# Kernel tuning notes

Measured on AMD Instinct MI355X. Metric: run time of the kernel, lower is better.

Reference implementation:

```python
import jax, jax.numpy as jnp
import numpy as np

D = 1024
HEADS = 16
HD = D // HEADS


def setup_inputs() -> dict:
    key = jax.random.key(0)
    kx, kqkv, kout = jax.random.split(key, 3)
    x = jax.random.normal(kx, (2, 2048, D), dtype=jnp.float32)
    # torch Linear weight is [out, in]; store same layout
    W_qkv = jax.random.normal(kqkv, (3 * D, D), dtype=jnp.float32) * (D ** -0.5)
    W_out = jax.random.normal(kout, (D, D), dtype=jnp.float32) * (D ** -0.5)
    return {"x": x, "W_qkv": W_qkv, "W_out": W_out}


def reference(x, W_qkv, W_out):
    B, T, _ = x.shape
    scale = HD ** -0.5
    qkv = jnp.einsum('btd,ed->bte', x, W_qkv)            # [B,T,3D]
    qkv = qkv.reshape(B, T, 3, HEADS, HD)
    q = jnp.transpose(qkv[:, :, 0], (0, 2, 1, 3))        # [B,H,T,hd]
    k = jnp.transpose(qkv[:, :, 1], (0, 2, 1, 3))
    v = jnp.transpose(qkv[:, :, 2], (0, 2, 1, 3))
    attn = jnp.einsum('bhqd,bhkd->bhqk', q, k) * scale   # [B,H,T,T]
    causal = jnp.tril(jnp.ones((T, T), dtype=bool))
    attn = jnp.where(causal, attn, -jnp.inf)
    attn = jax.nn.softmax(attn, axis=-1)
    out = jnp.einsum('bhqk,bhkd->bhqd', attn, v)         # [B,H,T,hd]
    out = jnp.transpose(out, (0, 2, 1, 3)).reshape(B, T, HEADS * HD)
    return jnp.einsum('btd,ed->bte', out, W_out)
```

## Files before the change

### kernel.cpp

```cpp
#include <hip/hip_runtime.h>
#include <cmath>


typedef unsigned short u16;
typedef unsigned int u32;
typedef short short8 __attribute__((ext_vector_type(8)));
typedef float floatx4 __attribute__((ext_vector_type(4)));

#define T_SZ 2048
#define HD_SZ 64
#define QSCALE 0.1803368801111244f

__device__ __forceinline__ u16 f2bf(float f) {
  unsigned u = __float_as_uint(f);
  u += 0x7fffu + ((u >> 16) & 1u);
  return (u16)(u >> 16);
}

__device__ __forceinline__ u32 pack_bf2(float lo, float hi) {
  return __builtin_amdgcn_perm(__float_as_uint(hi), __float_as_uint(lo), 0x07060302u);
}

__device__ __forceinline__ u32 cvtpk(float a, float b) {
  u32 r;
  asm("v_cvt_pk_bf16_f32 %0, %1, %2" : "=v"(r) : "v"(a), "v"(b));
  return r;
}

__device__ __forceinline__ void pl32swap(u32& a, u32& b) {
  asm("v_permlane32_swap_b32 %0, %1" : "+v"(a), "+v"(b));
}
__device__ __forceinline__ void pl16swap(u32& a, u32& b) {
  asm("v_permlane16_swap_b32 %0, %1" : "+v"(a), "+v"(b));
}

__device__ __forceinline__ void exp4(float s0, float s1, float s2, float s3,
                                     float& p0, float& p1, float& p2, float& p3) {
  asm("v_exp_f32 %0, %4\n\t"
      "v_exp_f32 %1, %5\n\t"
      "v_exp_f32 %2, %6\n\t"
      "v_exp_f32 %3, %7\n\t"
      "s_nop 1"
      : "=&v"(p0), "=&v"(p1), "=&v"(p2), "=&v"(p3)
      : "v"(s0), "v"(s1), "v"(s2), "v"(s3));
}

__device__ __forceinline__ void gload16(const u16* g, u16* l) {
  __builtin_amdgcn_global_load_lds(
      (const __attribute__((address_space(1))) void*)g,
      (__attribute__((address_space(3))) void*)l, 16, 0, 0);
}

__global__ __launch_bounds__(256) void cast3(const float* __restrict__ a, u16* __restrict__ ao, int na4,
                                             const float* __restrict__ b, u16* __restrict__ bo, int nb4,
                                             const float* __restrict__ c, u16* __restrict__ co, int nc4) {
  int i = blockIdx.x * 256 + threadIdx.x;
  const float* src;
  u16* dst;
  int j;
  if (i < na4) { src = a; dst = ao; j = i; }
  else if (i < na4 + nb4) { src = b; dst = bo; j = i - na4; }
  else { j = i - na4 - nb4; if (j >= nc4) return; src = c; dst = co; }
  float4 f = ((const float4*)src)[j];
  ushort4 o;
  o.x = f2bf(f.x); o.y = f2bf(f.y); o.z = f2bf(f.z); o.w = f2bf(f.w);
  ((ushort4*)dst)[j] = o;
}

__global__ __launch_bounds__(512, 6) void gemm_qkv(const u16* __restrict__ A,
                                                   const u16* __restrict__ Bt,
                                                   u16* __restrict__ Qf,
                                                   u16* __restrict__ Kf,
                                                   u16* __restrict__ Vf) {
  __shared__ u16 SM[4 * 64 * 72];
  u16* As = SM;
  u16* Bs = SM + 128 * 64;
  const int Kdim = 1024;
  const int tid = threadIdx.x;
  const int lane = tid & 63;
  const int wave = tid >> 6;
  const int quad = lane >> 4;
  const int l16 = lane & 15;
  const int wm = wave >> 2;
  const int wn = wave & 3;
  const int linear = blockIdx.y * 24 + blockIdx.x;
  const int nb = (linear & 7) * 96 + (linear >> 3);
  const int bxx = nb % 24;
  const int byy = nb / 24;
  const int m0 = byy * 128;
  const int n0 = bxx * 128;

  floatx4 acc[4][2];
#pragma unroll
  for (int i = 0; i < 4; i++)
#pragma unroll
    for (int j = 0; j < 2; j++) acc[i][j] = (floatx4){0.f, 0.f, 0.f, 0.f};

  const int srow = lane >> 3;
  const int scol = ((lane & 7) ^ srow) * 8;
  const u16* gpA[2];
  const u16* gpB[2];
  u16 *lpA[2], *lpB[2];
#pragma unroll
  for (int u = 0; u < 2; u++) {
    const int row = wave * 16 + u * 8 + srow;
    gpA[u] = A + (size_t)(m0 + row) * Kdim + scol;
    gpB[u] = Bt + (size_t)(n0 + row) * Kdim + scol;
    lpA[u] = As + (wave * 16 + u * 8) * 64 + lane * 8;
    lpB[u] = Bs + (wave * 16 + u * 8) * 64 + lane * 8;
  }

  const int fsw = l16 & 7;

  for (int k0 = 0; k0 < Kdim; k0 += 64) {
    __syncthreads();
#pragma unroll
    for (int u = 0; u < 2; u++) {
      gload16(gpA[u] + k0, lpA[u]);
      gload16(gpB[u] + k0, lpB[u]);
    }
    __syncthreads();

#pragma unroll
    for (int h = 0; h < 2; h++) {
      const int seg = ((h * 4 + quad) ^ fsw) * 8;
      short8 af[4], bf[2];
#pragma unroll
      for (int mt = 0; mt < 4; mt++)
        af[mt] = *(const short8*)&As[(wm * 64 + mt * 16 + l16) * 64 + seg];
#pragma unroll
      for (int nt = 0; nt < 2; nt++)
        bf[nt] = *(const short8*)&Bs[(wn * 32 + nt * 16 + l16) * 64 + seg];
#pragma unroll
      for (int mt = 0; mt < 4; mt++)
#pragma unroll
        for (int nt = 0; nt < 2; nt++)
          acc[mt][nt] = __builtin_amdgcn_mfma_f32_16x16x32_bf16(af[mt], bf[nt], acc[mt][nt], 0, 0, 0);
    }
  }

  const int dest = n0 >> 10;
  const int qn = wn >> 1;
  const int wh = wn & 1;
  const int n0w = n0 + qn * 64;
  const int m_abs = m0 + wm * 64;
  const int b = m_abs >> 11;
  const int t0w = m_abs & 2047;
  const int h = (n0w >> 6) & 15;
  const int bh = b * 16 + h;
  u16* dstp = (dest == 0) ? Qf : (dest == 1) ? Kf : Vf;

  __syncthreads();
  u16* ep = &SM[(wm * 2 + qn) * 64 * 72];
  if (dest == 2) {
#pragma unroll
    for (int nt = 0; nt < 2; nt++) {
#pragma unroll
      for (int mt = 0; mt < 4; mt++) {
        uint2 w;
        w.x = (u32)f2bf(acc[mt][nt][0]) | ((u32)f2bf(acc[mt][nt][1]) << 16);
        w.y = (u32)f2bf(acc[mt][nt][2]) | ((u32)f2bf(acc[mt][nt][3]) << 16);
        *(uint2*)&ep[(wh * 32 + nt * 16 + l16) * 72 + mt * 16 + quad * 4] = w;
      }
    }
  } else {
    const float sc = (dest == 0) ? QSCALE : 1.0f;
#pragma unroll
    for (int mt = 0; mt < 4; mt++)
#pragma unroll
      for (int nt = 0; nt < 2; nt++)
#pragma unroll
        for (int r = 0; r < 4; r++)
          ep[(mt * 16 + quad * 4 + r) * 72 + wh * 32 + nt * 16 + l16] =
              f2bf(acc[mt][nt][r] * sc);
  }
  __syncthreads();
#pragma unroll
  for (int blk = 0; blk < 4; blk++) {
    const int blkk = blk * 2 + wh;
    const int tgd = blkk >> 1;
    const int half = blkk & 1;
    const short8 v = *(const short8*)&ep[(tgd * 16 + l16) * 72 + half * 32 + quad * 8];
    size_t base;
    if (dest == 0)
      base = ((size_t)(bh * 128 + (t0w >> 4) + tgd) * 2 + half) * 512;
    else
      base = (((size_t)(bh * 32 + (t0w >> 6)) * 4 + tgd) * 2 + half) * 512;
    *(short8*)(dstp + base + lane * 8) = v;
  }
}

__global__ __launch_bounds__(512, 4) void gemm_out(const u16* __restrict__ A,
                                                   const u16* __restrict__ Bt,
                                                   float* __restrict__ Cout) {
  __shared__ u16 As[64 * 64];
  __shared__ u16 Bs[128 * 64];
  const int Kdim = 1024;
  const int tid = threadIdx.x;
  const int lane = tid & 63;
  const int wave = tid >> 6;
  const int quad = lane >> 4;
  const int l16 = lane & 15;
  const int wm = wave >> 2;
  const int wn = wave & 3;
  const int linear = blockIdx.y * 8 + blockIdx.x;
  const int nb = (linear & 7) * 64 + (linear >> 3);
  const int m0 = (nb >> 3) * 64;
  const int n0 = (nb & 7) * 128;

  floatx4 acc[2][2];
#pragma unroll
  for (int i = 0; i < 2; i++)
#pragma unroll
    for (int j = 0; j < 2; j++) acc[i][j] = (floatx4){0.f, 0.f, 0.f, 0.f};

  const int srow = lane >> 3;
  const int scol = ((lane & 7) ^ srow) * 8;
  const u16* gpA = A + (size_t)(m0 + wave * 8 + srow) * Kdim + scol;
  u16* lpA = As + (wave * 8) * 64 + lane * 8;
  const u16* gpB[2];
  u16* lpB[2];
#pragma unroll
  for (int u = 0; u < 2; u++) {
    const int row = wave * 16 + u * 8 + srow;
    gpB[u] = Bt + (size_t)(n0 + row) * Kdim + scol;
    lpB[u] = Bs + (wave * 16 + u * 8) * 64 + lane * 8;
  }

  const int fsw = l16 & 7;

  for (int k0 = 0; k0 < Kdim; k0 += 64) {
    __syncthreads();
    gload16(gpA + k0, lpA);
#pragma unroll
    for (int u = 0; u < 2; u++) gload16(gpB[u] + k0, lpB[u]);
    __syncthreads();

#pragma unroll
    for (int h = 0; h < 2; h++) {
      const int seg = ((h * 4 + quad) ^ fsw) * 8;
      short8 af[2], bf[2];
#pragma unroll
      for (int mt = 0; mt < 2; mt++)
        af[mt] = *(const short8*)&As[(wm * 32 + mt * 16 + l16) * 64 + seg];
#pragma unroll
      for (int nt = 0; nt < 2; nt++)
        bf[nt] = *(const short8*)&Bs[(wn * 32 + nt * 16 + l16) * 64 + seg];
#pragma unroll
      for (int mt = 0; mt < 2; mt++)
#pragma unroll
        for (int nt = 0; nt < 2; nt++)
          acc[mt][nt] = __builtin_amdgcn_mfma_f32_16x16x32_bf16(af[mt], bf[nt], acc[mt][nt], 0, 0, 0);
    }
  }

#pragma unroll
  for (int mt = 0; mt < 2; mt++)
#pragma unroll
    for (int nt = 0; nt < 2; nt++)
#pragma unroll
      for (int r = 0; r < 4; r++) {
        const int m = m0 + wm * 32 + mt * 16 + quad * 4 + r;
        const int n = n0 + wn * 32 + nt * 16 + l16;
        Cout[(size_t)m * 1024 + n] = acc[mt][nt][r];
      }
}

__global__ __launch_bounds__(256, 4) void flash_attn(const u16* __restrict__ Qf,
                                                     const u16* __restrict__ Kf,
                                                     const u16* __restrict__ Vf,
                                                     u16* __restrict__ Og) {
  __shared__ __align__(16) u16 KV[2][16 * 512];
  const int tid = threadIdx.x;
  const int lane = tid & 63, wave = tid >> 6;
  const int quad = lane >> 4, l16 = lane & 15;
  const int bh = blockIdx.x;
  const int by = blockIdx.y;
  const int r = by & 7, qq = by >> 3;
  const int g = (qq == 0) ? r : (qq == 1) ? 15 - r : (qq == 2) ? 16 + r : 31 - r;
  const int b = bh >> 4, h = bh & 15;
  const u16* Qb = Qf + ((size_t)bh << 17);
  const u16* Kb = Kf + ((size_t)bh << 17);
  const u16* Vb = Vf + ((size_t)bh << 17);

  const u16* qp = Qb + ((size_t)(g * 4 + wave)) * 1024 + lane * 8;
  const short8 qf0 = *(const short8*)qp;
  const short8 qf1 = *(const short8*)(qp + 512);

  floatx4 l_acc = (floatx4){0.f, 0.f, 0.f, 0.f};
  floatx4 o_acc[4];
#pragma unroll
  for (int dt = 0; dt < 4; dt++) o_acc[dt] = (floatx4){0.f, 0.f, 0.f, 0.f};

  short8 onesf;
#pragma unroll
  for (int i = 0; i < 8; i++) onesf[i] = (short)0x3F80;

  const u16* gkv[4];
  u16* l0[4];
  u16* l1[4];
#pragma unroll
  for (int i = 0; i < 4; i++) {
    const int c = wave * 4 + i;
    gkv[i] = ((c < 8) ? (Kb + c * 512) : (Vb + (c - 8) * 512)) + lane * 8;
    l0[i] = &KV[0][c * 512] + lane * 8;
    l1[i] = &KV[1][c * 512] + lane * 8;
  }

  auto load_tile = [&](int kt, u16* const* lp) {
#pragma unroll
    for (int i = 0; i < 4; i++) gload16(gkv[i] + (size_t)kt * 4096, lp[i]);
  };

  const floatx4 zero4 = {0.f, 0.f, 0.f, 0.f};

  auto compute = [&](int kt, const u16* Kl) {
    const bool diag = (kt == g);
    short8 ka[4][2];
#pragma unroll
    for (int nt = 0; nt < 4; nt++)
#pragma unroll
      for (int hh = 0; hh < 2; hh++)
        ka[nt][hh] = *(const short8*)&Kl[(nt * 2 + hh) * 512 + lane * 8];
    floatx4 sacc[4];
    __builtin_amdgcn_s_setprio(1);
#pragma unroll
    for (int nt = 0; nt < 4; nt++) {
      if (diag && nt > wave) continue;
      floatx4 s = __builtin_amdgcn_mfma_f32_16x16x32_bf16(ka[nt][0], qf0, zero4, 0, 0, 0);
      sacc[nt] = __builtin_amdgcn_mfma_f32_16x16x32_bf16(ka[nt][1], qf1, s, 0, 0, 0);
    }
    __builtin_amdgcn_s_setprio(0);
    u32 c[4][2];
#pragma unroll
    for (int nt = 0; nt < 4; nt++) {
      float p0 = 0.f, p1 = 0.f, p2 = 0.f, p3 = 0.f;
      if (!(diag && nt > wave)) {
        exp4(sacc[nt][0], sacc[nt][1], sacc[nt][2], sacc[nt][3], p0, p1, p2, p3);
        if (diag && nt == wave) {
          if (quad * 4 + 0 > l16) p0 = 0.f;
          if (quad * 4 + 1 > l16) p1 = 0.f;
          if (quad * 4 + 2 > l16) p2 = 0.f;
          if (quad * 4 + 3 > l16) p3 = 0.f;
        }
      }
      c[nt][0] = cvtpk(p0, p1);
      c[nt][1] = cvtpk(p2, p3);
    }
    pl32swap(c[0][0], c[1][0]); pl16swap(c[0][0], c[1][0]);
    pl32swap(c[0][1], c[1][1]); pl16swap(c[0][1], c[1][1]);
    pl32swap(c[2][0], c[3][0]); pl16swap(c[2][0], c[3][0]);
    pl32swap(c[2][1], c[3][1]); pl16swap(c[2][1], c[3][1]);
    union { u32 w[4]; short8 s8; } P0, P1;
    P0.w[0] = c[0][0]; P0.w[1] = c[0][1]; P0.w[2] = c[1][0]; P0.w[3] = c[1][1];
    P1.w[0] = c[2][0]; P1.w[1] = c[2][1]; P1.w[2] = c[3][0]; P1.w[3] = c[3][1];
    const short8 pf0 = P0.s8;
    const short8 pf1 = P1.s8;
    short8 va[4][2];
#pragma unroll
    for (int dt = 0; dt < 4; dt++)
#pragma unroll
      for (int hh = 0; hh < 2; hh++)
        va[dt][hh] = *(const short8*)&Kl[4096 + (dt * 2 + hh) * 512 + lane * 8];
    const bool skip_hi = diag && (wave < 2);
    __builtin_amdgcn_s_setprio(1);
    l_acc = __builtin_amdgcn_mfma_f32_16x16x32_bf16(onesf, pf0, l_acc, 0, 0, 0);
    if (!skip_hi)
      l_acc = __builtin_amdgcn_mfma_f32_16x16x32_bf16(onesf, pf1, l_acc, 0, 0, 0);
#pragma unroll
    for (int dt = 0; dt < 4; dt++) {
      o_acc[dt] = __builtin_amdgcn_mfma_f32_16x16x32_bf16(va[dt][0], pf0, o_acc[dt], 0, 0, 0);
      if (!skip_hi)
        o_acc[dt] = __builtin_amdgcn_mfma_f32_16x16x32_bf16(va[dt][1], pf1, o_acc[dt], 0, 0, 0);
    }
    __builtin_amdgcn_s_setprio(0);
  };

  load_tile(0, l0);
  __syncthreads();
  int kt = 0;
  for (;;) {
    if (kt < g) load_tile(kt + 1, l1);
    compute(kt, &KV[0][0]);
    if (++kt > g) break;
    __syncthreads();
    if (kt < g) load_tile(kt + 1, l0);
    compute(kt, &KV[1][0]);
    if (++kt > g) break;
    __syncthreads();
  }

  const float inv_l = 1.0f / l_acc[0];
  const int t0 = g * 64 + wave * 16;
  const size_t row = ((size_t)(b * 2048 + t0 + l16) << 10) + h * 64;
#pragma unroll
  for (int dt = 0; dt < 4; dt++) {
    uint2 w;
    w.x = pack_bf2(o_acc[dt][0] * inv_l, o_acc[dt][1] * inv_l);
    w.y = pack_bf2(o_acc[dt][2] * inv_l, o_acc[dt][3] * inv_l);
    *(uint2*)&Og[row + dt * 16 + quad * 4] = w;
  }
}

extern "C" void kernel_launch(void* const* d_in, const int* in_sizes, int n_in,
                              void* d_out, int out_size, void* d_ws, size_t ws_size,
                              hipStream_t stream) {
  const float* x = (const float*)d_in[0];
  const float* Wqkv = (const float*)d_in[1];
  const float* Wout = (const float*)d_in[2];
  float* out = (float*)d_out;

  char* ws = (char*)d_ws;
  u16* xb    = (u16*)(ws + 0);
  u16* wqkvb = (u16*)(ws + 8388608);
  u16* woutb = (u16*)(ws + 14680064);
  u16* Qf    = (u16*)(ws + 16777216);
  u16* Kf    = (u16*)(ws + 25165824);
  u16* Vf    = (u16*)(ws + 33554432);
  u16* attn  = (u16*)(ws + 41943040);

  cast3<<<8192, 256, 0, stream>>>(x, xb, 1048576, Wqkv, wqkvb, 786432,
                                  Wout, woutb, 262144);

  gemm_qkv<<<dim3(24, 32), 512, 0, stream>>>(xb, wqkvb, Qf, Kf, Vf);

  flash_attn<<<dim3(32, 32), 256, 0, stream>>>(Qf, Kf, Vf, attn);

  gemm_out<<<dim3(8, 64), 512, 0, stream>>>(attn, woutb, out);
}
```

Baseline: 154.7 us.

## Fuse cast, QKV GEMM, attention and output GEMM into one cooperative kernel

Replaces the four separate launches with a single persistent cooperative kernel of 1024 blocks of 256 threads. The stages are separated by grid.sync and keep the original multi-kernel path as a fallback. The GEMM stages are re-tiled for 256-thread blocks: the QKV GEMM keeps 128x128 tiles spread over 768 blocks, and the output GEMM uses smaller 64x64 tiles. The aim is to remove launch gaps and inter-kernel tail effects. The cost is grid-wide barriers, a 4-blocks-per-CU occupancy requirement, and smaller or different tiles that may lower GEMM efficiency.

```diff
diff --git a/kernel.cpp b/kernel.cpp
--- a/kernel.cpp
+++ b/kernel.cpp
@@ -1,5 +1,8 @@
 #include <hip/hip_runtime.h>
+#include <hip/hip_cooperative_groups.h>
 #include <cmath>
+
+namespace cg = cooperative_groups;
 
 
 typedef unsigned short u16;
@@ -7,8 +10,6 @@
 typedef short short8 __attribute__((ext_vector_type(8)));
 typedef float floatx4 __attribute__((ext_vector_type(4)));
 
-#define T_SZ 2048
-#define HD_SZ 64
 #define QSCALE 0.1803368801111244f
 
 __device__ __forceinline__ u16 f2bf(float f) {
@@ -49,6 +50,352 @@
   __builtin_amdgcn_global_load_lds(
       (const __attribute__((address_space(1))) void*)g,
       (__attribute__((address_space(3))) void*)l, 16, 0, 0);
+}
+
+__global__ __launch_bounds__(256, 4) void fused(const float* __restrict__ x,
+                                                const float* __restrict__ Wqkv,
+                                                const float* __restrict__ Wout,
+                                                u16* __restrict__ xb,
+                                                u16* __restrict__ wqkvb,
+                                                u16* __restrict__ woutb,
+                                                u16* __restrict__ Qf,
+                                                u16* __restrict__ Kf,
+                                                u16* __restrict__ Vf,
+                                                u16* __restrict__ attn,
+                                                float* __restrict__ out) {
+  cg::grid_group grid = cg::this_grid();
+  __shared__ __align__(16) u16 SM[2 * 128 * 64];
+
+  const int tid = threadIdx.x;
+  const int blk = blockIdx.x;
+  const int lane = tid & 63, wave = tid >> 6;
+  const int quad = lane >> 4, l16 = lane & 15;
+  const int srow = lane >> 3;
+  const int scol = ((lane & 7) ^ srow) * 8;
+  const int fsw = l16 & 7;
+
+  {
+    const int na4 = 1048576, nb4 = 786432, nc4 = 262144;
+    const int nTot = na4 + nb4 + nc4;
+    for (int i = blk * 256 + tid; i < nTot; i += 1024 * 256) {
+      const float* src;
+      u16* dst;
+      int j;
+      if (i < na4) { src = x; dst = xb; j = i; }
+      else if (i < na4 + nb4) { src = Wqkv; dst = wqkvb; j = i - na4; }
+      else { src = Wout; dst = woutb; j = i - na4 - nb4; }
+      float4 f = ((const float4*)src)[j];
+      ushort4 o;
+      o.x = f2bf(f.x); o.y = f2bf(f.y); o.z = f2bf(f.z); o.w = f2bf(f.w);
+      ((ushort4*)dst)[j] = o;
+    }
+  }
+  grid.sync();
+
+  if (blk < 768) {
+    u16* As = SM;
+    u16* Bs = SM + 128 * 64;
+    const int Kdim = 1024;
+    const int wm = wave >> 1, wn = wave & 1;
+    const int nb = (blk & 7) * 96 + (blk >> 3);
+    const int bxx = nb % 24;
+    const int byy = nb / 24;
+    const int m0 = byy * 128;
+    const int n0 = bxx * 128;
+
+    floatx4 acc[4][4];
+#pragma unroll
+    for (int i = 0; i < 4; i++)
+#pragma unroll
+      for (int j = 0; j < 4; j++) acc[i][j] = (floatx4){0.f, 0.f, 0.f, 0.f};
+
+    const u16* gpA[4];
+    const u16* gpB[4];
+    u16 *lpA[4], *lpB[4];
+#pragma unroll
+    for (int u = 0; u < 4; u++) {
+      const int row = wave * 32 + u * 8 + srow;
+      gpA[u] = xb + (size_t)(m0 + row) * Kdim + scol;
+      gpB[u] = wqkvb + (size_t)(n0 + row) * Kdim + scol;
+      lpA[u] = As + (wave * 32 + u * 8) * 64 + lane * 8;
+      lpB[u] = Bs + (wave * 32 + u * 8) * 64 + lane * 8;
+    }
+
+    for (int k0 = 0; k0 < Kdim; k0 += 64) {
+      __syncthreads();
+#pragma unroll
+      for (int u = 0; u < 4; u++) {
+        gload16(gpA[u] + k0, lpA[u]);
+        gload16(gpB[u] + k0, lpB[u]);
+      }
+      __syncthreads();
+#pragma unroll
+      for (int h = 0; h < 2; h++) {
+        const int seg = ((h * 4 + quad) ^ fsw) * 8;
+        short8 af[4], bf[4];
+#pragma unroll
+        for (int mt = 0; mt < 4; mt++)
+          af[mt] = *(const short8*)&As[(wm * 64 + mt * 16 + l16) * 64 + seg];
+#pragma unroll
+        for (int nt = 0; nt < 4; nt++)
+          bf[nt] = *(const short8*)&Bs[(wn * 64 + nt * 16 + l16) * 64 + seg];
+#pragma unroll
+        for (int mt = 0; mt < 4; mt++)
+#pragma unroll
+          for (int nt = 0; nt < 4; nt++)
+            acc[mt][nt] = __builtin_amdgcn_mfma_f32_16x16x32_bf16(af[mt], bf[nt], acc[mt][nt], 0, 0, 0);
+      }
+    }
+
+    const int dest = n0 >> 10;
+    const int n0w = n0 + wn * 64;
+    const int m_abs = m0 + wm * 64;
+    const int bb = m_abs >> 11;
+    const int t0w = m_abs & 2047;
+    const int hh_ = (n0w >> 6) & 15;
+    const int bh1 = bb * 16 + hh_;
+    u16* dstp = (dest == 0) ? Qf : (dest == 1) ? Kf : Vf;
+
+    auto do_epi = [&](u16* ep) {
+      if (dest == 2) {
+#pragma unroll
+        for (int nt = 0; nt < 4; nt++) {
+#pragma unroll
+          for (int mt = 0; mt < 4; mt++) {
+            uint2 w;
+            w.x = (u32)f2bf(acc[mt][nt][0]) | ((u32)f2bf(acc[mt][nt][1]) << 16);
+            w.y = (u32)f2bf(acc[mt][nt][2]) | ((u32)f2bf(acc[mt][nt][3]) << 16);
+            *(uint2*)&ep[(nt * 16 + l16) * 72 + mt * 16 + quad * 4] = w;
+          }
+        }
+      } else {
+        const float sc = (dest == 0) ? QSCALE : 1.0f;
+#pragma unroll
+        for (int mt = 0; mt < 4; mt++)
+#pragma unroll
+          for (int nt = 0; nt < 4; nt++)
+#pragma unroll
+            for (int r2 = 0; r2 < 4; r2++)
+              ep[(mt * 16 + quad * 4 + r2) * 72 + nt * 16 + l16] =
+                  f2bf(acc[mt][nt][r2] * sc);
+      }
+#pragma unroll
+      for (int bki = 0; bki < 8; bki++) {
+        const int tgd = bki >> 1;
+        const int half = bki & 1;
+        const short8 v = *(const short8*)&ep[(tgd * 16 + l16) * 72 + half * 32 + quad * 8];
+        size_t base;
+        if (dest == 0)
+          base = ((size_t)(bh1 * 128 + (t0w >> 4) + tgd) * 2 + half) * 512;
+        else
+          base = (((size_t)(bh1 * 32 + (t0w >> 6)) * 4 + tgd) * 2 + half) * 512;
+        *(short8*)(dstp + base + lane * 8) = v;
+      }
+    };
+
+    __syncthreads();
+    if (wave < 2) do_epi(&SM[wave * 64 * 72]);
+    __syncthreads();
+    if (wave >= 2) do_epi(&SM[(wave - 2) * 64 * 72]);
+  }
+  grid.sync();
+
+  {
+    u16* KV0 = SM;
+    u16* KV1 = SM + 16 * 512;
+    const int bh = blk & 31;
+    const int by = blk >> 5;
+    const int r = by & 7, qq = by >> 3;
+    const int g = (qq == 0) ? r : (qq == 1) ? 15 - r : (qq == 2) ? 16 + r : 31 - r;
+    const int b = bh >> 4, h = bh & 15;
+    const u16* Qb = Qf + ((size_t)bh << 17);
+    const u16* Kb = Kf + ((size_t)bh << 17);
+    const u16* Vb = Vf + ((size_t)bh << 17);
+
+    const u16* qp = Qb + ((size_t)(g * 4 + wave)) * 1024 + lane * 8;
+    const short8 qf0 = *(const short8*)qp;
+    const short8 qf1 = *(const short8*)(qp + 512);
+
+    floatx4 l_acc = (floatx4){0.f, 0.f, 0.f, 0.f};
+    floatx4 o_acc[4];
+#pragma unroll
+    for (int dt = 0; dt < 4; dt++) o_acc[dt] = (floatx4){0.f, 0.f, 0.f, 0.f};
+
+    short8 onesf;
+#pragma unroll
+    for (int i = 0; i < 8; i++) onesf[i] = (short)0x3F80;
+
+    const u16* gkv[4];
+    u16* l0[4];
+    u16* l1[4];
+#pragma unroll
+    for (int i = 0; i < 4; i++) {
+      const int c = wave * 4 + i;
+      gkv[i] = ((c < 8) ? (Kb + c * 512) : (Vb + (c - 8) * 512)) + lane * 8;
+      l0[i] = KV0 + c * 512 + lane * 8;
+      l1[i] = KV1 + c * 512 + lane * 8;
+    }
+
+    auto load_tile = [&](int kt, u16* const* lp) {
+#pragma unroll
+      for (int i = 0; i < 4; i++) gload16(gkv[i] + (size_t)kt * 4096, lp[i]);
+    };
+
+    const floatx4 zero4 = {0.f, 0.f, 0.f, 0.f};
+
+    auto compute = [&](int kt, const u16* Kl) {
+      const bool diag = (kt == g);
+      short8 ka[4][2];
+#pragma unroll
+      for (int nt = 0; nt < 4; nt++)
+#pragma unroll
+        for (int hh = 0; hh < 2; hh++)
+          ka[nt][hh] = *(const short8*)&Kl[(nt * 2 + hh) * 512 + lane * 8];
+      floatx4 sacc[4];
+      __builtin_amdgcn_s_setprio(1);
+#pragma unroll
+      for (int nt = 0; nt < 4; nt++) {
+        if (diag && nt > wave) continue;
+        floatx4 s = __builtin_amdgcn_mfma_f32_16x16x32_bf16(ka[nt][0], qf0, zero4, 0, 0, 0);
+        sacc[nt] = __builtin_amdgcn_mfma_f32_16x16x32_bf16(ka[nt][1], qf1, s, 0, 0, 0);
+      }
+      __builtin_amdgcn_s_setprio(0);
+      u32 c[4][2];
+#pragma unroll
+      for (int nt = 0; nt < 4; nt++) {
+        float p0 = 0.f, p1 = 0.f, p2 = 0.f, p3 = 0.f;
+        if (!(diag && nt > wave)) {
+          exp4(sacc[nt][0], sacc[nt][1], sacc[nt][2], sacc[nt][3], p0, p1, p2, p3);
+          if (diag && nt == wave) {
+            if (quad * 4 + 0 > l16) p0 = 0.f;
+            if (quad * 4 + 1 > l16) p1 = 0.f;
+            if (quad * 4 + 2 > l16) p2 = 0.f;
+            if (quad * 4 + 3 > l16) p3 = 0.f;
+          }
+        }
+        c[nt][0] = cvtpk(p0, p1);
+        c[nt][1] = cvtpk(p2, p3);
+      }
+      pl32swap(c[0][0], c[1][0]); pl16swap(c[0][0], c[1][0]);
+      pl32swap(c[0][1], c[1][1]); pl16swap(c[0][1], c[1][1]);
+      pl32swap(c[2][0], c[3][0]); pl16swap(c[2][0], c[3][0]);
+      pl32swap(c[2][1], c[3][1]); pl16swap(c[2][1], c[3][1]);
+      union { u32 w[4]; short8 s8; } P0, P1;
+      P0.w[0] = c[0][0]; P0.w[1] = c[0][1]; P0.w[2] = c[1][0]; P0.w[3] = c[1][1];
+      P1.w[0] = c[2][0]; P1.w[1] = c[2][1]; P1.w[2] = c[3][0]; P1.w[3] = c[3][1];
+      const short8 pf0 = P0.s8;
+      const short8 pf1 = P1.s8;
+      short8 va[4][2];
+#pragma unroll
+      for (int dt = 0; dt < 4; dt++)
+#pragma unroll
+        for (int hh = 0; hh < 2; hh++)
+          va[dt][hh] = *(const short8*)&Kl[4096 + (dt * 2 + hh) * 512 + lane * 8];
+      const bool skip_hi = diag && (wave < 2);
+      __builtin_amdgcn_s_setprio(1);
+      l_acc = __builtin_amdgcn_mfma_f32_16x16x32_bf16(onesf, pf0, l_acc, 0, 0, 0);
+      if (!skip_hi)
+        l_acc = __builtin_amdgcn_mfma_f32_16x16x32_bf16(onesf, pf1, l_acc, 0, 0, 0);
+#pragma unroll
+      for (int dt = 0; dt < 4; dt++) {
+        o_acc[dt] = __builtin_amdgcn_mfma_f32_16x16x32_bf16(va[dt][0], pf0, o_acc[dt], 0, 0, 0);
+        if (!skip_hi)
+          o_acc[dt] = __builtin_amdgcn_mfma_f32_16x16x32_bf16(va[dt][1], pf1, o_acc[dt], 0, 0, 0);
+      }
+      __builtin_amdgcn_s_setprio(0);
+    };
+
+    load_tile(0, l0);
+    __syncthreads();
+    int kt = 0;
+    for (;;) {
+      if (kt < g) load_tile(kt + 1, l1);
+      compute(kt, KV0);
+      if (++kt > g) break;
+      __syncthreads();
+      if (kt < g) load_tile(kt + 1, l0);
+      compute(kt, KV1);
+      if (++kt > g) break;
+      __syncthreads();
+    }
+
+    const float inv_l = 1.0f / l_acc[0];
+    const int t0 = g * 64 + wave * 16;
+    const size_t row = ((size_t)(b * 2048 + t0 + l16) << 10) + h * 64;
+#pragma unroll
+    for (int dt = 0; dt < 4; dt++) {
+      uint2 w;
+      w.x = pack_bf2(o_acc[dt][0] * inv_l, o_acc[dt][1] * inv_l);
+      w.y = pack_bf2(o_acc[dt][2] * inv_l, o_acc[dt][3] * inv_l);
+      *(uint2*)&attn[row + dt * 16 + quad * 4] = w;
+    }
+  }
+  grid.sync();
+
+  {
+    u16* As = SM;
+    u16* Bs = SM + 64 * 64;
+    const int Kdim = 1024;
+    const int wm = wave >> 1, wn = wave & 1;
+    const int nb = (blk & 7) * 128 + (blk >> 3);
+    const int m0 = (nb >> 4) * 64;
+    const int n0 = (nb & 15) * 64;
+
+    floatx4 acc[2][2];
+#pragma unroll
+    for (int i = 0; i < 2; i++)
+#pragma unroll
+      for (int j = 0; j < 2; j++) acc[i][j] = (floatx4){0.f, 0.f, 0.f, 0.f};
+
+    const u16* gpA[2];
+    const u16* gpB[2];
+    u16 *lpA[2], *lpB[2];
+#pragma unroll
+    for (int u = 0; u < 2; u++) {
+      const int row = wave * 16 + u * 8 + srow;
+      gpA[u] = attn + (size_t)(m0 + row) * Kdim + scol;
+      gpB[u] = woutb + (size_t)(n0 + row) * Kdim + scol;
+      lpA[u] = As + (wave * 16 + u * 8) * 64 + lane * 8;
+      lpB[u] = Bs + (wave * 16 + u * 8) * 64 + lane * 8;
+    }
+
+    for (int k0 = 0; k0 < Kdim; k0 += 64) {
+      __syncthreads();
+#pragma unroll
+      for (int u = 0; u < 2; u++) {
+        gload16(gpA[u] + k0, lpA[u]);
+        gload16(gpB[u] + k0, lpB[u]);
+      }
+      __syncthreads();
+#pragma unroll
+      for (int h = 0; h < 2; h++) {
+        const int seg = ((h * 4 + quad) ^ fsw) * 8;
+        short8 af[2], bf[2];
+#pragma unroll
+        for (int mt = 0; mt < 2; mt++)
+          af[mt] = *(const short8*)&As[(wm * 32 + mt * 16 + l16) * 64 + seg];
+#pragma unroll
+        for (int nt = 0; nt < 2; nt++)
+          bf[nt] = *(const short8*)&Bs[(wn * 32 + nt * 16 + l16) * 64 + seg];
+#pragma unroll
+        for (int mt = 0; mt < 2; mt++)
+#pragma unroll
+          for (int nt = 0; nt < 2; nt++)
+            acc[mt][nt] = __builtin_amdgcn_mfma_f32_16x16x32_bf16(af[mt], bf[nt], acc[mt][nt], 0, 0, 0);
+      }
+    }
+
+#pragma unroll
+    for (int mt = 0; mt < 2; mt++)
+#pragma unroll
+      for (int nt = 0; nt < 2; nt++)
+#pragma unroll
+        for (int r2 = 0; r2 < 4; r2++) {
+          const int m = m0 + wm * 32 + mt * 16 + quad * 4 + r2;
+          const int n = n0 + wn * 32 + nt * 16 + l16;
+          out[(size_t)m * 1024 + n] = acc[mt][nt][r2];
+        }
+  }
 }
 
 __global__ __launch_bounds__(256) void cast3(const float* __restrict__ a, u16* __restrict__ ao, int na4,
@@ -419,12 +766,21 @@
   u16* Vf    = (u16*)(ws + 33554432);
   u16* attn  = (u16*)(ws + 41943040);
 
+  int occ = 0;
+  hipError_t qerr = hipOccupancyMaxActiveBlocksPerMultiprocessor(&occ, fused, 256, 0);
+  if (qerr == hipSuccess && occ >= 4) {
+    void* args[] = {(void*)&x, (void*)&Wqkv, (void*)&Wout,
+                    (void*)&xb, (void*)&wqkvb, (void*)&woutb,
+                    (void*)&Qf, (void*)&Kf, (void*)&Vf,
+                    (void*)&attn, (void*)&out};
+    hipError_t lerr = hipLaunchCooperativeKernel(fused, dim3(1024), dim3(256),
+                                                 args, 0u, stream);
+    if (lerr == hipSuccess) return;
+  }
+
   cast3<<<8192, 256, 0, stream>>>(x, xb, 1048576, Wqkv, wqkvb, 786432,
                                   Wout, woutb, 262144);
-
   gemm_qkv<<<dim3(24, 32), 512, 0, stream>>>(xb, wqkvb, Qf, Kf, Vf);
-
   flash_attn<<<dim3(32, 32), 256, 0, stream>>>(Qf, Kf, Vf, attn);
-
   gemm_out<<<dim3(8, 64), 512, 0, stream>>>(attn, woutb, out);
 }
```

Result: no change. 157.4 us (+1.8%).
